# Kernel tuning notes

Hardware: AMD Instinct MI355X
Metric: run time of the kernel (lower is better)

Reference implementation:

```python
import jax, jax.numpy as jnp
import numpy as np

N = 8192
BOX = 50.0
CUTOFF = 5.0
MAX_E = 64 * N  # padded edge capacity (~34 avg neighbors expected)


def setup_inputs() -> dict:
    key = jax.random.key(0)
    pos = jax.random.uniform(key, (N, 3), dtype=jnp.float32) * BOX
    return {"pos": pos}


def _pairwise_dist(pos):
    # Euclidean cdist via the gram-matrix identity; avoids the [N,N,3] intermediate.
    sq = jnp.sum(pos * pos, axis=-1)                      # [N]
    d2 = sq[:, None] + sq[None, :] - 2.0 * (pos @ pos.T)  # [N,N]
    return jnp.sqrt(jnp.maximum(d2, 0.0))


def reference(pos):
    n = pos.shape[0]
    dist = _pairwise_dist(pos)
    # mask self-edges by pushing the diagonal above the cutoff (as in the torch code)
    dist = dist + (CUTOFF + 1.0) * jnp.eye(n, dtype=dist.dtype)
    mask = dist < CUTOFF
    # data-dependent nonzero -> fixed-size padded output for jit compatibility;
    # padded entries are filled with -1.
    rows, cols = jnp.nonzero(mask, size=MAX_E, fill_value=-1)
    return jnp.stack([rows, cols], axis=0)  # [2, MAX_E], int32
```

## Files before the change

kernel.cpp:

```cpp
#include <hip/hip_runtime.h>
#include <stdint.h>

#define N 8192
#define MAX_E (64 * N)
#define NCHUNK (N / 64)
#define NCOL1 9
#define NCOLS (NCOL1 * NCOL1)
#define CAP 256
#define SCALE (9.0f / 50.0f)
#define POISON 0xAAAAAAAAu
#define M_WAVES 4
#define E_BLOCKS 512
#define E_ROWS 16

__device__ __forceinline__ float sq_exact(float x, float y, float z) {
    return __fadd_rn(__fadd_rn(__fmul_rn(x, x), __fmul_rn(y, y)), __fmul_rn(z, z));
}

__device__ __forceinline__ bool edge_pred(float xi, float yi, float zi, float sqi,
                                          const float4& pj) {
    float dot = __fmaf_rn(zi, pj.z, __fmaf_rn(yi, pj.y, __fmul_rn(xi, pj.x)));
    float d2  = __fmaf_rn(-2.0f, dot, __fadd_rn(sqi, pj.w));
    return d2 < 0x1.8ffffep+4f;
}

__device__ __forceinline__ int cell_of(float v) {
    int c = (int)(__fmul_rn(v, SCALE));
    return c > 8 ? 8 : c;
}

__global__ __launch_bounds__(256) void bin_kernel(const float* __restrict__ posf,
                                                  unsigned* __restrict__ gcount,
                                                  float4* __restrict__ colpts,
                                                  int* __restrict__ colidx) {
    const int i = blockIdx.x * 256 + threadIdx.x;
    float x = posf[3 * i], y = posf[3 * i + 1], z = posf[3 * i + 2];
    int col = cell_of(x) * NCOL1 + cell_of(y);
    unsigned p = atomicAdd(&gcount[col], 1u) - POISON;
    if (p < CAP) {
        colpts[col * CAP + p] = make_float4(x, y, z, sq_exact(x, y, z));
        colidx[col * CAP + p] = i;
    }
}

__global__ __launch_bounds__(256) void mask_kernel(const float* __restrict__ posf,
                                                   const unsigned* __restrict__ gcount,
                                                   const float4* __restrict__ colpts,
                                                   const int* __restrict__ colidx,
                                                   uint64_t* __restrict__ masks,
                                                   int* __restrict__ counts) {
    __shared__ uint32_t lmask[M_WAVES][256];
    const int tid  = threadIdx.x;
    const int wave = tid >> 6;
    const int lane = tid & 63;
    const int row  = blockIdx.x * M_WAVES + wave;

#pragma unroll
    for (int k = lane; k < 256; k += 64) lmask[wave][k] = 0;

    const float xi = posf[3 * row], yi = posf[3 * row + 1], zi = posf[3 * row + 2];
    const float sqi = sq_exact(xi, yi, zi);
    const int cx = cell_of(xi), cy = cell_of(yi);
    __syncthreads();

    for (int dx = -1; dx <= 1; dx++) {
        const int nx = cx + dx;
        if ((unsigned)nx > 8u) continue;
        for (int dy = -1; dy <= 1; dy++) {
            const int ny = cy + dy;
            if ((unsigned)ny > 8u) continue;
            const int col = nx * NCOL1 + ny;
            int cnt = (int)(gcount[col] - POISON);
            if (cnt > CAP) cnt = CAP;
            for (int base = 0; base < cnt; base += 64) {
                const int k = base + lane;
                if (k < cnt) {
                    float4 pj = colpts[col * CAP + k];
                    int j = colidx[col * CAP + k];
                    if (j != row && edge_pred(xi, yi, zi, sqi, pj))
                        atomicOr(&lmask[wave][j >> 5], 1u << (j & 31));
                }
            }
        }
    }
    __syncthreads();

    uint4 u = ((const uint4*)lmask[wave])[lane];
    uint64_t k0 = (uint64_t)u.x | ((uint64_t)u.y << 32);
    uint64_t k1 = (uint64_t)u.z | ((uint64_t)u.w << 32);
    ulonglong2 v; v.x = k0; v.y = k1;
    ((ulonglong2*)(masks + (size_t)row * NCHUNK))[lane] = v;
    int t = __popcll(k0) + __popcll(k1);
#pragma unroll
    for (int o = 32; o > 0; o >>= 1) t += __shfl_down(t, o);
    if (lane == 0) counts[row] = t;
}

__global__ __launch_bounds__(256) void emit_kernel(const uint64_t* __restrict__ masks,
                                                   const int* __restrict__ counts,
                                                   int* __restrict__ out) {
    const int tid  = threadIdx.x;
    const int wave = tid >> 6;
    const int lane = tid & 63;
    const int row0 = blockIdx.x * E_ROWS;

    __shared__ int part[256];
    __shared__ int excl32[32];

    const int4* c4 = (const int4*)counts;
    int s = 0;
#pragma unroll
    for (int k = 0; k < 8; k++) {
        int4 v = c4[tid * 8 + k];
        s += v.x + v.y + v.z + v.w;
    }
    part[tid] = s;
    const int ch = row0 >> 5;
    if (tid < 32) excl32[tid] = counts[(ch << 5) + tid];
    __syncthreads();
    for (int off = 1; off < 256; off <<= 1) {
        int v = (tid >= off) ? part[tid - off] : 0;
        __syncthreads();
        part[tid] += v;
        __syncthreads();
    }
    if (tid == 0) {
        int run = 0;
#pragma unroll
        for (int k = 0; k < 32; k++) { int c = excl32[k]; excl32[k] = run; run += c; }
    }
    __syncthreads();
    const int base = (ch > 0) ? part[ch - 1] : 0;
    const int E    = part[255];
    const int sub  = row0 & 31;

    for (int idx = E + blockIdx.x * 256 + tid; idx < MAX_E; idx += E_BLOCKS * 256) {
        out[idx] = -1; out[MAX_E + idx] = -1;
    }

#pragma unroll
    for (int r = 0; r < 4; r++) {
        const int lr  = wave * 4 + r;
        const int row = row0 + lr;
        ulonglong2 v = ((const ulonglong2*)(masks + (size_t)row * NCHUNK))[lane];
        int s0 = __popcll(v.x), s1 = __popcll(v.y);
        int x = s0 + s1;
#pragma unroll
        for (int o = 1; o < 64; o <<= 1) {
            int t = __shfl_up(x, o);
            if (lane >= o) x += t;
        }
        int slot = base + excl32[sub + lr] + (x - (s0 + s1));

        const int col0 = lane * 128;
        uint64_t m = v.x;
        while (m) {
            int b = __ffsll((unsigned long long)m) - 1;
            m &= m - 1;
            if (slot < MAX_E) { out[slot] = row; out[MAX_E + slot] = col0 + b; }
            slot++;
        }
        m = v.y;
        while (m) {
            int b = __ffsll((unsigned long long)m) - 1;
            m &= m - 1;
            if (slot < MAX_E) { out[slot] = row; out[MAX_E + slot] = col0 + 64 + b; }
            slot++;
        }
    }
}

extern "C" void kernel_launch(void* const* d_in, const int* in_sizes, int n_in,
                              void* d_out, int out_size, void* d_ws, size_t ws_size,
                              hipStream_t stream) {
    const float* posf = (const float*)d_in[0];
    int* out = (int*)d_out;
    char* ws = (char*)d_ws;
    int*      counts = (int*)ws;
    unsigned* gcount = (unsigned*)(ws + (64 << 10));
    int*      colidx = (int*)(ws + (128 << 10));
    float4*   colpts = (float4*)(ws + (256 << 10));
    uint64_t* masks  = (uint64_t*)(ws + (1 << 20));

    bin_kernel<<<N / 256, 256, 0, stream>>>(posf, gcount, colpts, colidx);
    mask_kernel<<<N / M_WAVES, 256, 0, stream>>>(posf, gcount, colpts, colidx,
                                                 masks, counts);
    emit_kernel<<<E_BLOCKS, 256, 0, stream>>>(masks, counts, out);
}
```

Baseline: 86.91 us.

## Bin points into 3D cells, move -1 fill to mask kernel, use shuffle scans

Changes the spatial binning from 2D columns to 3D cells with a small per-cell capacity, so each row tests only the 27 neighbouring cells instead of 9 full-height columns. This sharply reduces candidate distance tests. The -1 padding fill moves into the mask kernel, which overwrites the whole output before emit writes edges. Block syncs become wave barriers, and emit's LDS Hillis-Steele scan becomes a wave-shuffle scan with 32 rows per block. Risks: a CAP of 40 per cell could overflow on denser inputs and silently drop edges, and correctness now relies on the fill finishing before emit runs.

```diff
diff --git a/kernel.cpp b/kernel.cpp
--- a/kernel.cpp
+++ b/kernel.cpp
@@ -5,13 +5,13 @@
 #define MAX_E (64 * N)
 #define NCHUNK (N / 64)
 #define NCOL1 9
-#define NCOLS (NCOL1 * NCOL1)
-#define CAP 256
+#define NCELLS (NCOL1 * NCOL1 * NCOL1)
+#define CAP 40
 #define SCALE (9.0f / 50.0f)
 #define POISON 0xAAAAAAAAu
 #define M_WAVES 4
-#define E_BLOCKS 512
-#define E_ROWS 16
+#define E_BLOCKS 256
+#define E_ROWS 32
 
 __device__ __forceinline__ float sq_exact(float x, float y, float z) {
     return __fadd_rn(__fadd_rn(__fmul_rn(x, x), __fmul_rn(y, y)), __fmul_rn(z, z));
@@ -27,6 +27,10 @@
 __device__ __forceinline__ int cell_of(float v) {
     int c = (int)(__fmul_rn(v, SCALE));
     return c > 8 ? 8 : c;
+}
+
+__device__ __forceinline__ int cell3_of(float x, float y, float z) {
+    return (cell_of(x) * NCOL1 + cell_of(y)) * NCOL1 + cell_of(z);
 }
 
 __global__ __launch_bounds__(256) void bin_kernel(const float* __restrict__ posf,
@@ -35,11 +39,11 @@
                                                   int* __restrict__ colidx) {
     const int i = blockIdx.x * 256 + threadIdx.x;
     float x = posf[3 * i], y = posf[3 * i + 1], z = posf[3 * i + 2];
-    int col = cell_of(x) * NCOL1 + cell_of(y);
-    unsigned p = atomicAdd(&gcount[col], 1u) - POISON;
+    const int cell = cell3_of(x, y, z);
+    unsigned p = atomicAdd(&gcount[cell], 1u) - POISON;
     if (p < CAP) {
-        colpts[col * CAP + p] = make_float4(x, y, z, sq_exact(x, y, z));
-        colidx[col * CAP + p] = i;
+        colpts[cell * CAP + p] = make_float4(x, y, z, sq_exact(x, y, z));
+        colidx[cell * CAP + p] = i;
     }
 }
 
@@ -48,20 +52,26 @@
                                                    const float4* __restrict__ colpts,
                                                    const int* __restrict__ colidx,
                                                    uint64_t* __restrict__ masks,
-                                                   int* __restrict__ counts) {
+                                                   int* __restrict__ counts,
+                                                   int* __restrict__ out) {
     __shared__ uint32_t lmask[M_WAVES][256];
     const int tid  = threadIdx.x;
     const int wave = tid >> 6;
     const int lane = tid & 63;
     const int row  = blockIdx.x * M_WAVES + wave;
 
+    int2 neg; neg.x = -1; neg.y = -1;
+    ((int2*)out)[blockIdx.x * 256 + tid] = neg;
+
 #pragma unroll
     for (int k = lane; k < 256; k += 64) lmask[wave][k] = 0;
+    __builtin_amdgcn_wave_barrier();
 
     const float xi = posf[3 * row], yi = posf[3 * row + 1], zi = posf[3 * row + 2];
     const float sqi = sq_exact(xi, yi, zi);
-    const int cx = cell_of(xi), cy = cell_of(yi);
-    __syncthreads();
+    const int cx = cell_of(xi), cy = cell_of(yi), cz = cell_of(zi);
+    const int zlo = (cz > 0) ? cz - 1 : 0;
+    const int zhi = (cz < 8) ? cz + 1 : 8;
 
     for (int dx = -1; dx <= 1; dx++) {
         const int nx = cx + dx;
@@ -69,21 +79,27 @@
         for (int dy = -1; dy <= 1; dy++) {
             const int ny = cy + dy;
             if ((unsigned)ny > 8u) continue;
-            const int col = nx * NCOL1 + ny;
-            int cnt = (int)(gcount[col] - POISON);
-            if (cnt > CAP) cnt = CAP;
-            for (int base = 0; base < cnt; base += 64) {
-                const int k = base + lane;
-                if (k < cnt) {
-                    float4 pj = colpts[col * CAP + k];
-                    int j = colidx[col * CAP + k];
-                    if (j != row && edge_pred(xi, yi, zi, sqi, pj))
-                        atomicOr(&lmask[wave][j >> 5], 1u << (j & 31));
-                }
+            const int c0 = (nx * NCOL1 + ny) * NCOL1 + zlo;
+            int l0 = (int)(gcount[c0] - POISON);     l0 = l0 > CAP ? CAP : l0;
+            int l1 = (int)(gcount[c0 + 1] - POISON); l1 = l1 > CAP ? CAP : l1;
+            int l2 = 0;
+            if (zhi - zlo == 2) {
+                l2 = (int)(gcount[c0 + 2] - POISON); l2 = l2 > CAP ? CAP : l2;
             }
-        }
-    }
-    __syncthreads();
+            const int t01 = l0 + l1;
+            const int tot = t01 + l2;
+            for (int k = lane; k < tot; k += 64) {
+                const int cellk = c0 + (k >= l0) + (k >= t01);
+                const int off = k - ((k >= l0) ? l0 : 0) - ((k >= t01) ? l1 : 0);
+                const int a = cellk * CAP + off;
+                float4 pj = colpts[a];
+                int j = colidx[a];
+                if (j != row && edge_pred(xi, yi, zi, sqi, pj))
+                    atomicOr(&lmask[wave][j >> 5], 1u << (j & 31));
+            }
+        }
+    }
+    __builtin_amdgcn_wave_barrier();
 
     uint4 u = ((const uint4*)lmask[wave])[lane];
     uint64_t k0 = (uint64_t)u.x | ((uint64_t)u.y << 32);
@@ -104,7 +120,8 @@
     const int lane = tid & 63;
     const int row0 = blockIdx.x * E_ROWS;
 
-    __shared__ int part[256];
+    __shared__ int incl[256];
+    __shared__ int wtot[4];
     __shared__ int excl32[32];
 
     const int4* c4 = (const int4*)counts;
@@ -114,43 +131,45 @@
         int4 v = c4[tid * 8 + k];
         s += v.x + v.y + v.z + v.w;
     }
-    part[tid] = s;
-    const int ch = row0 >> 5;
-    if (tid < 32) excl32[tid] = counts[(ch << 5) + tid];
+    int x = s;
+#pragma unroll
+    for (int o = 1; o < 64; o <<= 1) {
+        int t = __shfl_up(x, o);
+        if (lane >= o) x += t;
+    }
+    if (lane == 63) wtot[wave] = x;
+
+    if (tid < 32) {
+        int c = counts[row0 + tid];
+        int y = c;
+#pragma unroll
+        for (int o = 1; o < 32; o <<= 1) {
+            int t = __shfl_up(y, o, 32);
+            if (tid >= o) y += t;
+        }
+        excl32[tid] = y - c;
+    }
     __syncthreads();
-    for (int off = 1; off < 256; off <<= 1) {
-        int v = (tid >= off) ? part[tid - off] : 0;
-        __syncthreads();
-        part[tid] += v;
-        __syncthreads();
-    }
-    if (tid == 0) {
-        int run = 0;
-#pragma unroll
-        for (int k = 0; k < 32; k++) { int c = excl32[k]; excl32[k] = run; run += c; }
-    }
+    int woff = 0;
+#pragma unroll
+    for (int w = 0; w < 3; w++) woff += (wave > w) ? wtot[w] : 0;
+    incl[tid] = woff + x;
     __syncthreads();
-    const int base = (ch > 0) ? part[ch - 1] : 0;
-    const int E    = part[255];
-    const int sub  = row0 & 31;
-
-    for (int idx = E + blockIdx.x * 256 + tid; idx < MAX_E; idx += E_BLOCKS * 256) {
-        out[idx] = -1; out[MAX_E + idx] = -1;
-    }
-
-#pragma unroll
-    for (int r = 0; r < 4; r++) {
-        const int lr  = wave * 4 + r;
+    const int base = (blockIdx.x > 0) ? incl[blockIdx.x - 1] : 0;
+
+#pragma unroll
+    for (int r = 0; r < 8; r++) {
+        const int lr  = wave * 8 + r;
         const int row = row0 + lr;
         ulonglong2 v = ((const ulonglong2*)(masks + (size_t)row * NCHUNK))[lane];
         int s0 = __popcll(v.x), s1 = __popcll(v.y);
-        int x = s0 + s1;
+        int xs = s0 + s1;
 #pragma unroll
         for (int o = 1; o < 64; o <<= 1) {
-            int t = __shfl_up(x, o);
-            if (lane >= o) x += t;
-        }
-        int slot = base + excl32[sub + lr] + (x - (s0 + s1));
+            int t = __shfl_up(xs, o);
+            if (lane >= o) xs += t;
+        }
+        int slot = base + excl32[lr] + (xs - (s0 + s1));
 
         const int col0 = lane * 128;
         uint64_t m = v.x;
@@ -184,6 +203,6 @@
 
     bin_kernel<<<N / 256, 256, 0, stream>>>(posf, gcount, colpts, colidx);
     mask_kernel<<<N / M_WAVES, 256, 0, stream>>>(posf, gcount, colpts, colidx,
-                                                 masks, counts);
+                                                 masks, counts, out);
     emit_kernel<<<E_BLOCKS, 256, 0, stream>>>(masks, counts, out);
 }
```

Result: faster. 79.03 us (-9.1%).
